# Optimization experiments

Hardware: AMD Instinct MI355X
Metric: run time of the kernel (lower is better)

## Reference

```python
import jax, jax.numpy as jnp
import numpy as np

U, I, A, D, NC = 20000, 15000, 2048, 64, 2048
N = U + I
E_AU, E_AI, E_UI, E_R = 300000, 300000, 300000, 60000


def setup_inputs() -> dict:
    keys = iter(jax.random.split(jax.random.key(0), 128))
    def rn(shape, s=0.05):
        return jax.random.normal(next(keys), shape, jnp.float32) * s
    def ru(shape):
        return jax.random.uniform(next(keys), shape, dtype=jnp.float32)
    def ri(shape, mx):
        return jax.random.randint(next(keys), shape, 0, mx)
    d = {}
    for nm in ("feature1", "feature2", "feature3", "weight1", "weight2", "weight3", "weight4", "weight5"):
        d[nm] = rn((N, D))
    d["W_review1"] = rn((D, D)); d["W_review2"] = rn((D, D))
    for i in range(1, 7):
        d["rating_emb%d" % i] = rn((5, D))
    d["W_aspect"] = rn((D, D)); d["W_aspect2"] = rn((D, D))
    d["W_count_user"] = rn((NC, D)); d["b_count_user"] = rn((D,))
    d["W_count_item"] = rn((NC, D)); d["b_count_item"] = rn((D,))
    d["aspect_fe"] = rn((A, D)); d["aspect_cau"] = rn((A, D)); d["aspect_cai"] = rn((A, D))
    d["user_cau"] = rn((U, D)); d["user_cui"] = rn((U, D))
    d["item_cai"] = rn((I, D)); d["item_ciu"] = rn((I, D))
    for i in range(1, 6):
        d["user_cui%d" % i] = rn((U, D)); d["item_ciu%d" % i] = rn((I, D))
    d["user_mask"] = ru((U,)); d["item_mask"] = ru((I,))
    d["user_aspect_count"] = ru((U, NC)); d["item_aspect_count"] = ru((I, NC))
    d["ui_review"] = rn((E_UI, D), 1.0); d["iu_review"] = rn((E_UI, D), 1.0)
    for i in range(1, 6):
        d["ui%d_review" % i] = rn((E_R, D), 1.0); d["iu%d_review" % i] = rn((E_R, D), 1.0)
    d["au_src"] = ri((E_AU,), A); d["au_dst"] = ri((E_AU,), U)
    d["ai_src"] = ri((E_AI,), A); d["ai_dst"] = ri((E_AI,), I)
    d["ui_src"] = ri((E_UI,), U); d["ui_dst"] = ri((E_UI,), I); d["ui_rating"] = ri((E_UI,), 5)
    d["iu_src"] = ri((E_UI,), I); d["iu_dst"] = ri((E_UI,), U); d["iu_rating"] = ri((E_UI,), 5)
    for i in range(1, 6):
        d["ui%d_src" % i] = ri((E_R,), U); d["ui%d_dst" % i] = ri((E_R,), I)
        d["iu%d_src" % i] = ri((E_R,), I); d["iu%d_dst" % i] = ri((E_R,), U)
    return d


def reference(feature1, feature2, feature3, weight1, weight2, weight3, weight4, weight5,
              W_review1, W_review2, rating_emb1, rating_emb2, rating_emb3, rating_emb4,
              rating_emb5, rating_emb6, W_aspect, W_aspect2, W_count_user, b_count_user,
              W_count_item, b_count_item, aspect_fe, aspect_cau, aspect_cai,
              user_cau, user_cui, user_cui1, user_cui2, user_cui3, user_cui4, user_cui5,
              user_mask, user_aspect_count, item_cai, item_ciu, item_ciu1, item_ciu2,
              item_ciu3, item_ciu4, item_ciu5, item_mask, item_aspect_count,
              ui_review, iu_review, ui1_review, ui2_review, ui3_review, ui4_review, ui5_review,
              iu1_review, iu2_review, iu3_review, iu4_review, iu5_review,
              au_src, au_dst, ai_src, ai_dst, ui_src, ui_dst, ui_rating,
              iu_src, iu_dst, iu_rating,
              ui1_src, ui1_dst, ui2_src, ui2_dst, ui3_src, ui3_dst, ui4_src, ui4_dst,
              ui5_src, ui5_dst, iu1_src, iu1_dst, iu2_src, iu2_dst, iu3_src, iu3_dst,
              iu4_src, iu4_dst, iu5_src, iu5_dst):
    sig = jax.nn.sigmoid
    cat = jnp.concatenate
    def seg(m, idx, n):
        return jax.ops.segment_sum(m, idx, num_segments=n)
    u_fe1, i_fe1 = feature1[:U], feature1[U:]
    u_fe2, i_fe2 = feature2[:U], feature2[U:]
    u_fe3, i_fe3 = feature3[:U], feature3[U:]
    mu = user_mask[:, None]; mi = item_mask[:, None]
    # --- aspect -> user/item (dropout = identity, eval mode) ---
    f_fe = aspect_fe @ W_aspect        # [A, D]
    f_fe2 = aspect_fe @ W_aspect2
    h_u = seg((f_fe * aspect_cau)[au_src], au_dst, U)
    h_i = seg((f_fe2 * aspect_cai)[ai_src], ai_dst, I)
    from_a_u = mu * (h_u * user_cau) + (1.0 - mu) * u_fe2
    from_a_i = mi * (h_i * item_cai) + (1.0 - mi) * i_fe2
    # --- rating-gated pass over from_a ---
    h_i = seg((from_a_u * user_cui)[ui_src] * sig(rating_emb1[ui_rating]), ui_dst, I)
    h_u = seg((from_a_i * item_ciu)[iu_src] * sig(rating_emb2[iu_rating]), iu_dst, U)
    user_item_senti_fe = cat([h_u * user_cui, h_i * item_ciu], 0)
    # --- aspect-count pass ---
    ac_u = user_aspect_count @ W_count_user + b_count_user
    ac_i = item_aspect_count @ W_count_item + b_count_item
    ac_u = mu * (ac_u * user_cau) + (1.0 - mu) * u_fe3
    ac_i = mi * (ac_i * item_cai) + (1.0 - mi) * i_fe3
    h_i = seg((ac_u * user_cui)[ui_src] * sig(rating_emb3[ui_rating]), ui_dst, I)
    h_u = seg((ac_i * item_ciu)[iu_src] * sig(rating_emb4[iu_rating]), iu_dst, U)
    user_item_count_fe = cat([h_u * user_cui, h_i * item_ciu], 0)
    # --- per-rating relations ---
    ws = [weight1, weight2, weight3, weight4, weight5]
    cuis = [user_cui1, user_cui2, user_cui3, user_cui4, user_cui5]
    cius = [item_ciu1, item_ciu2, item_ciu3, item_ciu4, item_ciu5]
    ui_e = [(ui1_src, ui1_dst, ui1_review), (ui2_src, ui2_dst, ui2_review),
            (ui3_src, ui3_dst, ui3_review), (ui4_src, ui4_dst, ui4_review),
            (ui5_src, ui5_dst, ui5_review)]
    iu_e = [(iu1_src, iu1_dst, iu1_review), (iu2_src, iu2_dst, iu2_review),
            (iu3_src, iu3_dst, iu3_review), (iu4_src, iu4_dst, iu4_review),
            (iu5_src, iu5_dst, iu5_review)]
    fe5_parts, re_parts = [], []
    for w, cui_k, ciu_k, (us, ud, urv), (isrc, idst, irv) in zip(ws, cuis, cius, ui_e, iu_e):
        re_ui = urv @ W_review1        # [E_R, D]
        re_iu = irv @ W_review2
        wu, wi = w[:U], w[U:]
        h_ik = seg((wu[us] + re_ui) * cui_k[us], ud, I)
        h_uk = seg((wi[isrc] + re_iu) * ciu_k[isrc], idst, U)
        fe5_parts.append(cat([h_uk * cui_k, h_ik * ciu_k], 0))
        h_ir = seg(re_ui * cui_k[us], ud, I)
        h_ur = seg(re_iu * ciu_k[isrc], idst, U)
        re_parts.append(cat([h_ur * cui_k, h_ir * ciu_k], 0))
    user_item_fe5 = cat(fe5_parts, -1)   # [N, 5*D]
    user_item_re = cat(re_parts, -1)
    # --- base-feature pass ---
    h_i = seg((u_fe1 * user_cui)[ui_src] * sig(rating_emb5[ui_rating]), ui_dst, I)
    h_u = seg((i_fe1 * item_ciu)[iu_src] * sig(rating_emb6[iu_rating]), iu_dst, U)
    user_item_fe = cat([h_u * user_cui, h_i * item_ciu], 0)
    return (user_item_senti_fe, user_item_count_fe, user_item_fe, user_item_fe5, user_item_re)
```

## Files before the change

### kernel.cpp

```cpp
#include <hip/hip_runtime.h>
#include <cstddef>

#define U_CNT 20000
#define I_CNT 15000
#define N_CNT 35000
#define A_CNT 2048
#define NC_K  2048
#define EAU   300000
#define EUI   300000
#define ER    60000
#define NLIST 14

__device__ __forceinline__ float4 ld4(const float* p){ return *reinterpret_cast<const float4*>(p); }
__device__ __forceinline__ void st4(float* p, float4 v){ *reinterpret_cast<float4*>(p) = v; }
__device__ __forceinline__ float4 mul4(float4 a, float4 b){ return make_float4(a.x*b.x, a.y*b.y, a.z*b.z, a.w*b.w); }
__device__ __forceinline__ float4 add4(float4 a, float4 b){ return make_float4(a.x+b.x, a.y+b.y, a.z+b.z, a.w+b.w); }
__device__ __forceinline__ float4 fmas4(float s, float4 b, float4 c){
  return make_float4(fmaf(s,b.x,c.x), fmaf(s,b.y,c.y), fmaf(s,b.z,c.z), fmaf(s,b.w,c.w));
}

__global__ __launch_bounds__(256) void fill_m1(int4* __restrict__ p, int n4)
{
  int gid = blockIdx.x*256 + threadIdx.x;
  if (gid < n4) p[gid] = make_int4(-1,-1,-1,-1);
}

__device__ __forceinline__ void gemm_core(
    const float* __restrict__ A, int lda, int M, int r0,
    const float* __restrict__ W, int k0base, int kcount,
    float* __restrict__ smem, float4* accs)
{
  float (*As)[36] = (float (*)[36])smem;
  float (*Ws)[64] = (float (*)[64])(smem + 64*36);
  const int t = threadIdx.x;
  const int ty = t >> 4, tx = t & 15;
  float4 acc0 = make_float4(0,0,0,0), acc1 = acc0, acc2 = acc0, acc3 = acc0;
  for (int k0 = k0base; k0 < k0base + kcount; k0 += 32) {
    __syncthreads();
    #pragma unroll
    for (int i = 0; i < 2; ++i) {
      int f = t + i*256;
      int row = f >> 3, caa = (f & 7) << 2;
      float4 v = make_float4(0.f,0.f,0.f,0.f);
      int r = r0 + row;
      if (r < M) v = ld4(&A[(size_t)r*lda + k0 + caa]);
      st4(&As[row][caa], v);
      int kk = f >> 4, cb = (f & 15) << 2;
      st4(&Ws[kk][cb], ld4(&W[(size_t)(k0+kk)*64 + cb]));
    }
    __syncthreads();
    #pragma unroll
    for (int kk = 0; kk < 32; kk += 4) {
      float4 a0 = ld4(&As[ty*4+0][kk]);
      float4 a1 = ld4(&As[ty*4+1][kk]);
      float4 a2 = ld4(&As[ty*4+2][kk]);
      float4 a3 = ld4(&As[ty*4+3][kk]);
      float a0v[4] = {a0.x,a0.y,a0.z,a0.w};
      float a1v[4] = {a1.x,a1.y,a1.z,a1.w};
      float a2v[4] = {a2.x,a2.y,a2.z,a2.w};
      float a3v[4] = {a3.x,a3.y,a3.z,a3.w};
      #pragma unroll
      for (int j = 0; j < 4; ++j) {
        float4 wv = ld4(&Ws[kk+j][tx<<2]);
        acc0 = fmas4(a0v[j], wv, acc0);
        acc1 = fmas4(a1v[j], wv, acc1);
        acc2 = fmas4(a2v[j], wv, acc2);
        acc3 = fmas4(a3v[j], wv, acc3);
      }
    }
  }
  accs[0]=acc0; accs[1]=acc1; accs[2]=acc2; accs[3]=acc3;
}

struct Mega1Args {
  int e_sp, e_build, e_k64, e_fe1c, split;
  const float* emb[6]; float* sigt;
  const float* f1; const float* cui; const float* ciu; float* fe1c;
  const float* spA[2]; const float* spW[2]; float* spPart[2]; int spM[2];
  const float* kA[12]; const float* kW[12]; const float* kMul[12]; float* kC[12]; int kM[12];
  const int* bsrc[NLIST]; const int* bdst[NLIST];
  const int* rat2; const int* rat3;
  int2* node[NLIST]; int* head[NLIST];
};

__global__ __launch_bounds__(256, 8) void mega1(Mega1Args a)
{
  __shared__ float smem[64*36 + 32*64];
  int b = blockIdx.x, t = threadIdx.x;
  if (b < a.e_sp) {
    int nb0 = a.split*313;
    int side, sp, bx;
    if (b < nb0) { side = 0; sp = b/313; bx = b%313; }
    else         { int b2 = b-nb0; side = 1; sp = b2/235; bx = b2%235; }
    int M = a.spM[side];
    int r0 = bx*64;
    int kchunk = NC_K / a.split;
    float4 accs[4];
    gemm_core(a.spA[side], NC_K, M, r0, a.spW[side], sp*kchunk, kchunk, smem, accs);
    float* base = a.spPart[side] + (size_t)sp * M * 64;
    int ty = t >> 4, tx = t & 15;
    #pragma unroll
    for (int i = 0; i < 4; ++i) {
      int r = r0 + ty*4 + i;
      if (r < M) st4(&base[(size_t)r*64 + (tx<<2)], accs[i]);
    }
    return;
  }
  if (b < a.e_build) {
    int local = b - a.e_sp;
    int li, bx;
    if (local < 4*1172) { li = local/1172; bx = local%1172; }
    else { int l2 = local - 4*1172; li = 4 + l2/235; bx = l2%235; }
    int E = (li < 4) ? EAU : ER;
    int i = bx*256 + t;
    if (i < E) {
      int d = a.bdst[li][i];
      int pay = a.bsrc[li][i];
      if (li == 2) pay |= a.rat2[i] << 20;
      else if (li == 3) pay |= a.rat3[i] << 20;
      int prev = atomicExch(&a.head[li][d], i);
      a.node[li][i] = make_int2(prev, pay);
    }
    return;
  }
  if (b < a.e_k64) {
    int local = b - a.e_build;
    int z, bx;
    if (local < 64) { z = local/32; bx = local%32; }
    else { int l2 = local - 64; z = 2 + l2/938; bx = l2%938; }
    int M = a.kM[z];
    int r0 = bx*64;
    float4 accs[4];
    gemm_core(a.kA[z], 64, M, r0, a.kW[z], 0, 64, smem, accs);
    const float* mulp = a.kMul[z];
    float* C = a.kC[z];
    int ty = t >> 4, tx = t & 15;
    #pragma unroll
    for (int i = 0; i < 4; ++i) {
      int r = r0 + ty*4 + i;
      if (r < M) {
        float4 v = accs[i];
        size_t o = (size_t)r*64 + (tx<<2);
        if (mulp) v = mul4(v, ld4(&mulp[o]));
        st4(&C[o], v);
      }
    }
    return;
  }
  if (b < a.e_fe1c) {
    int gid = (b - a.e_k64)*256 + t;
    if (gid < N_CNT*16) {
      int n = gid >> 4, q = (gid & 15) << 2;
      size_t o = (size_t)n*64 + q;
      float4 v = ld4(&a.f1[o]);
      float4 c = (n < U_CNT) ? ld4(&a.cui[o]) : ld4(&a.ciu[(size_t)(n-U_CNT)*64 + q]);
      st4(&a.fe1c[o], mul4(v, c));
    }
    return;
  }
  {
    int gid = (b - a.e_fe1c)*256 + t;
    if (gid < 6*320) {
      int k = gid/320, j = gid%320;
      a.sigt[gid] = 1.f/(1.f + __expf(-a.emb[k][j]));
    }
  }
}

#define FE5Z 10
struct Mega2Args {
  int split;
  const int* f_head[FE5Z]; const int2* f_node[FE5Z];
  const float* f_re[FE5Z]; const float* f_w[FE5Z]; const float* f_cui[FE5Z];
  const float* f_cmul[FE5Z]; float* f_outA[FE5Z]; float* f_outB[FE5Z]; int f_n[FE5Z];
  const int* gb_head[2]; const int2* gb_node[2];
  const float* gb_msg[2]; const float* gb_mask[2]; const float* gb_ca[2];
  const float* gb_fe[2]; const float* gb_cui[2]; float* gb_out[2]; int gb_n[2];
  const float* part[2]; int M[2];
  const float* bias[2]; const float* mask[2];
  const float* ca[2]; const float* fe[2]; const float* cui[2]; float* outb[2];
};

__global__ __launch_bounds__(256) void mega2(Mega2Args a)
{
  int b = blockIdx.x, t = threadIdx.x;
  int q = (t & 15) << 2;
  const int B_FE5 = 5*1250 + 5*938;
  if (b < B_FE5) {
    int z, bx;
    if (b < 6250) { z = 2*(b/1250) + 1; bx = b%1250; }
    else { int l2 = b - 6250; z = 2*(l2/938); bx = l2%938; }
    int d = bx*16 + (t >> 4);
    if (d >= a.f_n[z]) return;
    const int2* __restrict__ node = a.f_node[z];
    const float* __restrict__ re = a.f_re[z];
    const float* __restrict__ w = a.f_w[z];
    const float* __restrict__ cuiS = a.f_cui[z];
    float4 a0 = make_float4(0,0,0,0), a1 = a0;
    for (int cur = a.f_head[z][d]; cur >= 0; ) {
      int2 nd = node[cur];
      int e = cur;
      cur = nd.x;
      int s = nd.y;
      float4 rv = ld4(&re[(size_t)e*64 + q]);
      float4 cv = ld4(&cuiS[(size_t)s*64 + q]);
      float4 wv = ld4(&w[(size_t)s*64 + q]);
      a0 = add4(a0, mul4(add4(wv, rv), cv));
      a1 = add4(a1, mul4(rv, cv));
    }
    float4 c = ld4(&a.f_cmul[z][(size_t)d*64 + q]);
    size_t o = (size_t)d*320 + q;
    st4(&a.f_outA[z][o], mul4(a0, c));
    st4(&a.f_outB[z][o], mul4(a1, c));
    return;
  }
  int local = b - B_FE5;
  if (local < 2188) {
    int side = (local >= 1250);
    int bx = side ? (local - 1250) : local;
    int d = bx*16 + (t >> 4);
    if (d >= a.gb_n[side]) return;
    const int2* __restrict__ node = a.gb_node[side];
    const float* __restrict__ msg = a.gb_msg[side];
    float4 acc = make_float4(0,0,0,0);
    for (int cur = a.gb_head[side][d]; cur >= 0; ) {
      int2 nd = node[cur];
      cur = nd.x;
      acc = add4(acc, ld4(&msg[(size_t)nd.y*64 + q]));
    }
    size_t o = (size_t)d*64 + q;
    float m = a.gb_mask[side][d], im = 1.f - m;
    float4 cav = ld4(&a.gb_ca[side][o]), fev = ld4(&a.gb_fe[side][o]), cv = ld4(&a.gb_cui[side][o]);
    st4(&a.gb_out[side][o], make_float4((m*(acc.x*cav.x) + im*fev.x)*cv.x,
                                        (m*(acc.y*cav.y) + im*fev.y)*cv.y,
                                        (m*(acc.z*cav.z) + im*fev.z)*cv.z,
                                        (m*(acc.w*cav.w) + im*fev.w)*cv.w));
    return;
  }
  local -= 2188;
  int side = (local >= 1250);
  int gid = (side ? (local - 1250) : local)*256 + t;
  int M = a.M[side];
  if (gid >= M*16) return;
  int n = gid >> 4;
  float4 acc = ld4(&a.bias[side][q]);
  const float* part = a.part[side];
  for (int s = 0; s < a.split; ++s)
    acc = add4(acc, ld4(&part[((size_t)s*M + n)*64 + q]));
  size_t o = (size_t)n*64 + q;
  float m = a.mask[side][n], im = 1.f - m;
  float4 cav = ld4(&a.ca[side][o]), fev = ld4(&a.fe[side][o]), cv = ld4(&a.cui[side][o]);
  st4(&a.outb[side][o], make_float4((m*(acc.x*cav.x) + im*fev.x)*cv.x,
                                    (m*(acc.y*cav.y) + im*fev.y)*cv.y,
                                    (m*(acc.z*cav.z) + im*fev.z)*cv.z,
                                    (m*(acc.w*cav.w) + im*fev.w)*cv.w));
}

struct Mega3Args {
  int e_g3i;
  const int* head[2]; const int2* node[2];
  const float* msgA[2]; const float* msgB[2]; const float* msgC[2];
  const float* sigA[2]; const float* sigB[2]; const float* sigC[2];
  const float* cmul[2]; float* outA[2]; float* outB[2]; float* outC[2]; int n[2];
};

__global__ __launch_bounds__(256) void mega3(Mega3Args a)
{
  int b = blockIdx.x, t = threadIdx.x;
  int side = (b >= a.e_g3i);
  int bx = side ? (b - a.e_g3i) : b;
  int d = bx*16 + (t >> 4);
  if (d >= a.n[side]) return;
  int q = (t & 15) << 2;
  const int2* __restrict__ node = a.node[side];
  const float* __restrict__ msgA = a.msgA[side];
  const float* __restrict__ msgB = a.msgB[side];
  const float* __restrict__ msgC = a.msgC[side];
  const float* __restrict__ sigA = a.sigA[side];
  const float* __restrict__ sigB = a.sigB[side];
  const float* __restrict__ sigC = a.sigC[side];
  float4 a0 = make_float4(0,0,0,0), a1 = a0, a2 = a0;
  for (int cur = a.head[side][d]; cur >= 0; ) {
    int2 nd = node[cur];
    cur = nd.x;
    int s = nd.y & 0xFFFFF;
    int r = nd.y >> 20;
    size_t so = (size_t)s*64 + q;
    int ro = r*64 + q;
    a0 = add4(a0, mul4(ld4(&msgA[so]), ld4(&sigA[ro])));
    a1 = add4(a1, mul4(ld4(&msgB[so]), ld4(&sigB[ro])));
    a2 = add4(a2, mul4(ld4(&msgC[so]), ld4(&sigC[ro])));
  }
  size_t o = (size_t)d*64 + q;
  float4 c = ld4(&a.cmul[side][o]);
  st4(&a.outA[side][o], mul4(a0, c));
  st4(&a.outB[side][o], mul4(a1, c));
  st4(&a.outC[side][o], mul4(a2, c));
}

extern "C" void kernel_launch(void* const* d_in, const int* in_sizes, int n_in,
                              void* d_out, int out_size, void* d_ws, size_t ws_size,
                              hipStream_t stream)
{
  (void)in_sizes; (void)n_in; (void)out_size;
  auto F = [&](int i){ return (const float*)d_in[i]; };
  auto Ix = [&](int i){ return (const int*)d_in[i]; };

  const float* feature1 = F(0);
  const float* feature2 = F(1);
  const float* feature3 = F(2);
  const float* weightK[5]   = {F(3),F(4),F(5),F(6),F(7)};
  const float* W_review1 = F(8);
  const float* W_review2 = F(9);
  const float* rating_emb[6] = {F(10),F(11),F(12),F(13),F(14),F(15)};
  const float* W_aspect  = F(16);
  const float* W_aspect2 = F(17);
  const float* W_count_user = F(18);
  const float* b_count_user = F(19);
  const float* W_count_item = F(20);
  const float* b_count_item = F(21);
  const float* aspect_fe  = F(22);
  const float* aspect_cau = F(23);
  const float* aspect_cai = F(24);
  const float* user_cau = F(25);
  const float* user_cui = F(26);
  const float* item_cai = F(27);
  const float* item_ciu = F(28);
  const float* user_cuiK[5] = {F(29),F(31),F(33),F(35),F(37)};
  const float* item_ciuK[5] = {F(30),F(32),F(34),F(36),F(38)};
  const float* user_mask = F(39);
  const float* item_mask = F(40);
  const float* user_aspect_count = F(41);
  const float* item_aspect_count = F(42);
  const float* uiK_review[5] = {F(45),F(47),F(49),F(51),F(53)};
  const float* iuK_review[5] = {F(46),F(48),F(50),F(52),F(54)};
  const int* au_src = Ix(55); const int* au_dst = Ix(56);
  const int* ai_src = Ix(57); const int* ai_dst = Ix(58);
  const int* ui_src = Ix(59); const int* ui_dst = Ix(60); const int* ui_rating = Ix(61);
  const int* iu_src = Ix(62); const int* iu_dst = Ix(63); const int* iu_rating = Ix(64);
  const int* uiK_src[5] = {Ix(65),Ix(69),Ix(73),Ix(77),Ix(81)};
  const int* uiK_dst[5] = {Ix(66),Ix(70),Ix(74),Ix(78),Ix(82)};
  const int* iuK_src[5] = {Ix(67),Ix(71),Ix(75),Ix(79),Ix(83)};
  const int* iuK_dst[5] = {Ix(68),Ix(72),Ix(76),Ix(80),Ix(84)};

  float* out  = (float*)d_out;
  float* out2 = out + (size_t)N_CNT*64;
  float* out3 = out + 2*(size_t)N_CNT*64;
  float* out4 = out + 3*(size_t)N_CNT*64;
  float* out5 = out + 8*(size_t)N_CNT*64;

  float* ws = (float*)d_ws;
  size_t off = 0;
  auto alloc = [&](size_t n){ float* p = ws + off; off += (n + 3) & ~(size_t)3; return p; };
  float* sigt   = alloc(6*320);
  float* msg_au = alloc((size_t)A_CNT*64);
  float* msg_ai = alloc((size_t)A_CNT*64);
  float* h_u_a  = alloc((size_t)U_CNT*64);
  float* h_i_a  = alloc((size_t)I_CNT*64);
  float* g_u    = alloc((size_t)U_CNT*64);
  float* g_i    = alloc((size_t)I_CNT*64);
  float* fe1c   = alloc((size_t)N_CNT*64);

  const int* l_src[NLIST] = {au_src, ai_src, ui_src, iu_src,
                             uiK_src[0],uiK_src[1],uiK_src[2],uiK_src[3],uiK_src[4],
                             iuK_src[0],iuK_src[1],iuK_src[2],iuK_src[3],iuK_src[4]};
  const int* l_dst[NLIST] = {au_dst, ai_dst, ui_dst, iu_dst,
                             uiK_dst[0],uiK_dst[1],uiK_dst[2],uiK_dst[3],uiK_dst[4],
                             iuK_dst[0],iuK_dst[1],iuK_dst[2],iuK_dst[3],iuK_dst[4]};
  int l_E[NLIST]    = {EAU,EAU,EUI,EUI, ER,ER,ER,ER,ER, ER,ER,ER,ER,ER};
  int l_nseg[NLIST] = {U_CNT,I_CNT,I_CNT,U_CNT, I_CNT,I_CNT,I_CNT,I_CNT,I_CNT,
                       U_CNT,U_CNT,U_CNT,U_CNT,U_CNT};

  int* ibase = (int*)(ws + off);
  int* lhead[NLIST]; int2* lnode[NLIST];
  size_t io = 0;
  for (int l = 0; l < NLIST; ++l) { lhead[l] = ibase + io; io += l_nseg[l]; }
  size_t head_ints = io;
  for (int l = 0; l < NLIST; ++l) { lnode[l] = (int2*)(ibase + io); io += 2*(size_t)l_E[l]; }
  off += (io + 3) & ~(size_t)3;

  const size_t reN = (size_t)ER*64;
  int SPLIT = 4;
  while (SPLIT > 1 && (off + (size_t)SPLIT*N_CNT*64 + 10*reN) * 4 > ws_size) SPLIT >>= 1;
  float* part_u = ws + off;
  float* part_i = part_u + (size_t)SPLIT*U_CNT*64;
  float* rebase = part_u + (size_t)SPLIT*N_CNT*64;
  float* reb[10];
  for (int j = 0; j < 10; ++j) reb[j] = rebase + (size_t)j*reN;

  fill_m1<<<(int)((head_ints/4 + 255)/256), 256, 0, stream>>>((int4*)ibase, (int)(head_ints/4));

  Mega1Args a1;
  const int B_SP    = SPLIT*313 + SPLIT*235;
  const int B_BUILD = 4*1172 + 10*235;
  const int B_K64   = 2*32 + 10*938;
  const int B_FE1C  = (N_CNT*16 + 255)/256;
  const int B_SIG   = 8;
  a1.e_sp    = B_SP;
  a1.e_build = B_SP + B_BUILD;
  a1.e_k64   = a1.e_build + B_K64;
  a1.e_fe1c  = a1.e_k64 + B_FE1C;
  a1.split   = SPLIT;
  for (int k = 0; k < 6; ++k) a1.emb[k] = rating_emb[k];
  a1.sigt = sigt;
  a1.f1 = feature1; a1.cui = user_cui; a1.ciu = item_ciu; a1.fe1c = fe1c;
  a1.spA[0] = user_aspect_count; a1.spW[0] = W_count_user; a1.spPart[0] = part_u; a1.spM[0] = U_CNT;
  a1.spA[1] = item_aspect_count; a1.spW[1] = W_count_item; a1.spPart[1] = part_i; a1.spM[1] = I_CNT;
  a1.kA[0]=aspect_fe; a1.kW[0]=W_aspect;  a1.kMul[0]=aspect_cau; a1.kC[0]=msg_au; a1.kM[0]=A_CNT;
  a1.kA[1]=aspect_fe; a1.kW[1]=W_aspect2; a1.kMul[1]=aspect_cai; a1.kC[1]=msg_ai; a1.kM[1]=A_CNT;
  for (int k = 0; k < 5; ++k) {
    a1.kA[2+k]=uiK_review[k]; a1.kW[2+k]=W_review1; a1.kMul[2+k]=nullptr; a1.kC[2+k]=reb[k];   a1.kM[2+k]=ER;
    a1.kA[7+k]=iuK_review[k]; a1.kW[7+k]=W_review2; a1.kMul[7+k]=nullptr; a1.kC[7+k]=reb[5+k]; a1.kM[7+k]=ER;
  }
  for (int l = 0; l < NLIST; ++l) {
    a1.bsrc[l]=l_src[l]; a1.bdst[l]=l_dst[l];
    a1.node[l]=lnode[l]; a1.head[l]=lhead[l];
  }
  a1.rat2 = ui_rating; a1.rat3 = iu_rating;
  mega1<<<a1.e_fe1c + B_SIG, 256, 0, stream>>>(a1);

  Mega2Args a2;
  a2.split = SPLIT;
  for (int k = 0; k < 5; ++k) {
    int z = 2*k;
    a2.f_head[z]=lhead[4+k]; a2.f_node[z]=lnode[4+k];
    a2.f_re[z]=reb[k]; a2.f_w[z]=weightK[k]; a2.f_cui[z]=user_cuiK[k]; a2.f_cmul[z]=item_ciuK[k];
    a2.f_outA[z]=out4 + (size_t)U_CNT*320 + (size_t)k*64;
    a2.f_outB[z]=out5 + (size_t)U_CNT*320 + (size_t)k*64;
    a2.f_n[z]=I_CNT;
    a2.f_head[z+1]=lhead[9+k]; a2.f_node[z+1]=lnode[9+k];
    a2.f_re[z+1]=reb[5+k]; a2.f_w[z+1]=weightK[k] + (size_t)U_CNT*64;
    a2.f_cui[z+1]=item_ciuK[k]; a2.f_cmul[z+1]=user_cuiK[k];
    a2.f_outA[z+1]=out4 + (size_t)k*64;
    a2.f_outB[z+1]=out5 + (size_t)k*64;
    a2.f_n[z+1]=U_CNT;
  }
  a2.gb_head[0]=lhead[0]; a2.gb_node[0]=lnode[0]; a2.gb_msg[0]=msg_au;
  a2.gb_mask[0]=user_mask; a2.gb_ca[0]=user_cau; a2.gb_fe[0]=feature2;
  a2.gb_cui[0]=user_cui; a2.gb_out[0]=h_u_a; a2.gb_n[0]=U_CNT;
  a2.gb_head[1]=lhead[1]; a2.gb_node[1]=lnode[1]; a2.gb_msg[1]=msg_ai;
  a2.gb_mask[1]=item_mask; a2.gb_ca[1]=item_cai; a2.gb_fe[1]=feature2 + (size_t)U_CNT*64;
  a2.gb_cui[1]=item_ciu; a2.gb_out[1]=h_i_a; a2.gb_n[1]=I_CNT;
  a2.part[0]=part_u; a2.M[0]=U_CNT; a2.bias[0]=b_count_user; a2.mask[0]=user_mask;
  a2.ca[0]=user_cau; a2.fe[0]=feature3; a2.cui[0]=user_cui; a2.outb[0]=g_u;
  a2.part[1]=part_i; a2.M[1]=I_CNT; a2.bias[1]=b_count_item; a2.mask[1]=item_mask;
  a2.ca[1]=item_cai; a2.fe[1]=feature3 + (size_t)U_CNT*64; a2.cui[1]=item_ciu; a2.outb[1]=g_i;
  const int B_M2 = (5*1250 + 5*938) + 2188 + 2188;
  mega2<<<B_M2, 256, 0, stream>>>(a2);

  Mega3Args a3;
  a3.e_g3i = 938;
  a3.head[0]=lhead[2]; a3.node[0]=lnode[2];
  a3.msgA[0]=h_u_a; a3.msgB[0]=g_u; a3.msgC[0]=fe1c;
  a3.sigA[0]=sigt + 0*320; a3.sigB[0]=sigt + 2*320; a3.sigC[0]=sigt + 4*320;
  a3.cmul[0]=item_ciu;
  a3.outA[0]=out + (size_t)U_CNT*64; a3.outB[0]=out2 + (size_t)U_CNT*64; a3.outC[0]=out3 + (size_t)U_CNT*64;
  a3.n[0]=I_CNT;
  a3.head[1]=lhead[3]; a3.node[1]=lnode[3];
  a3.msgA[1]=h_i_a; a3.msgB[1]=g_i; a3.msgC[1]=fe1c + (size_t)U_CNT*64;
  a3.sigA[1]=sigt + 1*320; a3.sigB[1]=sigt + 3*320; a3.sigC[1]=sigt + 5*320;
  a3.cmul[1]=user_cui;
  a3.outA[1]=out; a3.outB[1]=out2; a3.outC[1]=out3;
  a3.n[1]=U_CNT;
  mega3<<<938 + 1250, 256, 0, stream>>>(a3);
}
```

Before: 459.9 us.

## Use bf16x3 split MFMA for dense GEMMs with prepacked hi/lo weights

Replaces the shared-memory fp32 FMA GEMM core in mega1 with MFMA 16x16x32 bf16 instructions, using a three-term hi/lo bf16 split to keep close to fp32 accuracy. Weights are converted once per call in a new prep kernel, fused with the -1 fill, into an MFMA-friendly packed layout. Activations are split on the fly from global memory with no LDS staging, and the launch bounds are relaxed. The aim is to cut ALU time in the large count GEMM (U/I x 2048 x 64) and the review projections. The cost is three MFMAs per tile, scalar strided output stores, and a small loss of accuracy from dropping the lo*lo term.

Result: no change. 458.1 us (-0.4%).

```diff
diff --git a/kernel.cpp b/kernel.cpp
--- a/kernel.cpp
+++ b/kernel.cpp
@@ -11,81 +11,103 @@
 #define ER    60000
 #define NLIST 14
 
+typedef __attribute__((ext_vector_type(8))) short bf16x8;
+typedef __attribute__((ext_vector_type(4))) float f32x4;
+
 __device__ __forceinline__ float4 ld4(const float* p){ return *reinterpret_cast<const float4*>(p); }
 __device__ __forceinline__ void st4(float* p, float4 v){ *reinterpret_cast<float4*>(p) = v; }
 __device__ __forceinline__ float4 mul4(float4 a, float4 b){ return make_float4(a.x*b.x, a.y*b.y, a.z*b.z, a.w*b.w); }
 __device__ __forceinline__ float4 add4(float4 a, float4 b){ return make_float4(a.x+b.x, a.y+b.y, a.z+b.z, a.w+b.w); }
-__device__ __forceinline__ float4 fmas4(float s, float4 b, float4 c){
-  return make_float4(fmaf(s,b.x,c.x), fmaf(s,b.y,c.y), fmaf(s,b.z,c.z), fmaf(s,b.w,c.w));
-}
-
-__global__ __launch_bounds__(256) void fill_m1(int4* __restrict__ p, int n4)
-{
-  int gid = blockIdx.x*256 + threadIdx.x;
-  if (gid < n4) p[gid] = make_int4(-1,-1,-1,-1);
-}
-
-__device__ __forceinline__ void gemm_core(
+
+__device__ __forceinline__ void cvt_hilo(float4 a, float4 b, bf16x8& h, bf16x8& l)
+{
+  float v0=a.x,v1=a.y,v2=a.z,v3=a.w,v4=b.x,v5=b.y,v6=b.z,v7=b.w;
+  float vv[8] = {v0,v1,v2,v3,v4,v5,v6,v7};
+  #pragma unroll
+  for (int j = 0; j < 8; ++j) {
+    unsigned int bi = __float_as_uint(vv[j]);
+    h[j] = (short)(bi >> 16);
+    float hf = __uint_as_float(bi & 0xffff0000u);
+    l[j] = (short)(__float_as_uint(vv[j] - hf) >> 16);
+  }
+}
+
+__device__ __forceinline__ void gemm_mfma(
     const float* __restrict__ A, int lda, int M, int r0,
-    const float* __restrict__ W, int k0base, int kcount,
-    float* __restrict__ smem, float4* accs)
-{
-  float (*As)[36] = (float (*)[36])smem;
-  float (*Ws)[64] = (float (*)[64])(smem + 64*36);
+    const unsigned short* __restrict__ Wh, const unsigned short* __restrict__ Wl,
+    int s0, int nsteps, f32x4* acc)
+{
   const int t = threadIdx.x;
-  const int ty = t >> 4, tx = t & 15;
-  float4 acc0 = make_float4(0,0,0,0), acc1 = acc0, acc2 = acc0, acc3 = acc0;
-  for (int k0 = k0base; k0 < k0base + kcount; k0 += 32) {
-    __syncthreads();
+  const int w = t >> 6, l = t & 63;
+  const int lr = l & 15, g = l >> 4;
+  const int row = r0 + w*16 + lr;
+  const bool rowok = row < M;
+  const float* arow = A + (size_t)row*lda;
+  for (int s = s0; s < s0 + nsteps; ++s) {
+    float4 a0 = make_float4(0.f,0.f,0.f,0.f), a1 = a0;
+    if (rowok) {
+      a0 = ld4(arow + s*32 + g*8);
+      a1 = ld4(arow + s*32 + g*8 + 4);
+    }
+    bf16x8 ah, al;
+    cvt_hilo(a0, a1, ah, al);
+    const unsigned short* bh_base = Wh + (size_t)(s*4 + g)*64*8;
+    const unsigned short* bl_base = Wl + (size_t)(s*4 + g)*64*8;
     #pragma unroll
-    for (int i = 0; i < 2; ++i) {
-      int f = t + i*256;
-      int row = f >> 3, caa = (f & 7) << 2;
-      float4 v = make_float4(0.f,0.f,0.f,0.f);
-      int r = r0 + row;
-      if (r < M) v = ld4(&A[(size_t)r*lda + k0 + caa]);
-      st4(&As[row][caa], v);
-      int kk = f >> 4, cb = (f & 15) << 2;
-      st4(&Ws[kk][cb], ld4(&W[(size_t)(k0+kk)*64 + cb]));
-    }
-    __syncthreads();
-    #pragma unroll
-    for (int kk = 0; kk < 32; kk += 4) {
-      float4 a0 = ld4(&As[ty*4+0][kk]);
-      float4 a1 = ld4(&As[ty*4+1][kk]);
-      float4 a2 = ld4(&As[ty*4+2][kk]);
-      float4 a3 = ld4(&As[ty*4+3][kk]);
-      float a0v[4] = {a0.x,a0.y,a0.z,a0.w};
-      float a1v[4] = {a1.x,a1.y,a1.z,a1.w};
-      float a2v[4] = {a2.x,a2.y,a2.z,a2.w};
-      float a3v[4] = {a3.x,a3.y,a3.z,a3.w};
-      #pragma unroll
-      for (int j = 0; j < 4; ++j) {
-        float4 wv = ld4(&Ws[kk+j][tx<<2]);
-        acc0 = fmas4(a0v[j], wv, acc0);
-        acc1 = fmas4(a1v[j], wv, acc1);
-        acc2 = fmas4(a2v[j], wv, acc2);
-        acc3 = fmas4(a3v[j], wv, acc3);
-      }
-    }
-  }
-  accs[0]=acc0; accs[1]=acc1; accs[2]=acc2; accs[3]=acc3;
+    for (int cb = 0; cb < 4; ++cb) {
+      bf16x8 bh = *reinterpret_cast<const bf16x8*>(bh_base + (cb*16 + lr)*8);
+      bf16x8 bl = *reinterpret_cast<const bf16x8*>(bl_base + (cb*16 + lr)*8);
+      acc[cb] = __builtin_amdgcn_mfma_f32_16x16x32_bf16(ah, bh, acc[cb], 0, 0, 0);
+      acc[cb] = __builtin_amdgcn_mfma_f32_16x16x32_bf16(ah, bl, acc[cb], 0, 0, 0);
+      acc[cb] = __builtin_amdgcn_mfma_f32_16x16x32_bf16(al, bh, acc[cb], 0, 0, 0);
+    }
+  }
+}
+
+struct PrepArgs {
+  int e_fill;
+  int4* fillp; int fill_n4;
+  const float* wsrc[6]; unsigned short* whi[6]; unsigned short* wlo[6];
+  int welems[6]; int wblocks[6];
+};
+
+__global__ __launch_bounds__(256) void prep(PrepArgs a)
+{
+  int b = blockIdx.x, t = threadIdx.x;
+  if (b < a.e_fill) {
+    int gid = b*256 + t;
+    if (gid < a.fill_n4) a.fillp[gid] = make_int4(-1,-1,-1,-1);
+    return;
+  }
+  int local = b - a.e_fill;
+  int z = 0;
+  while (z < 5 && local >= a.wblocks[z]) { local -= a.wblocks[z]; ++z; }
+  int e = local*256 + t;
+  if (e >= a.welems[z]) return;
+  int k = e >> 6, c = e & 63;
+  int idx = ((k >> 3)*64 + c)*8 + (k & 7);
+  float v = a.wsrc[z][e];
+  unsigned int bi = __float_as_uint(v);
+  a.whi[z][idx] = (unsigned short)(bi >> 16);
+  float hf = __uint_as_float(bi & 0xffff0000u);
+  a.wlo[z][idx] = (unsigned short)(__float_as_uint(v - hf) >> 16);
 }
 
 struct Mega1Args {
   int e_sp, e_build, e_k64, e_fe1c, split;
   const float* emb[6]; float* sigt;
   const float* f1; const float* cui; const float* ciu; float* fe1c;
-  const float* spA[2]; const float* spW[2]; float* spPart[2]; int spM[2];
-  const float* kA[12]; const float* kW[12]; const float* kMul[12]; float* kC[12]; int kM[12];
+  const float* spA[2]; const unsigned short* spWh[2]; const unsigned short* spWl[2];
+  float* spPart[2]; int spM[2];
+  const float* kA[12]; const unsigned short* kWh[12]; const unsigned short* kWl[12];
+  const float* kMul[12]; float* kC[12]; int kM[12];
   const int* bsrc[NLIST]; const int* bdst[NLIST];
   const int* rat2; const int* rat3;
   int2* node[NLIST]; int* head[NLIST];
 };
 
-__global__ __launch_bounds__(256, 8) void mega1(Mega1Args a)
-{
-  __shared__ float smem[64*36 + 32*64];
+__global__ __launch_bounds__(256, 4) void mega1(Mega1Args a)
+{
   int b = blockIdx.x, t = threadIdx.x;
   if (b < a.e_sp) {
     int nb0 = a.split*313;
@@ -94,16 +116,21 @@
     else         { int b2 = b-nb0; side = 1; sp = b2/235; bx = b2%235; }
     int M = a.spM[side];
     int r0 = bx*64;
-    int kchunk = NC_K / a.split;
-    float4 accs[4];
-    gemm_core(a.spA[side], NC_K, M, r0, a.spW[side], sp*kchunk, kchunk, smem, accs);
+    int spsteps = NC_K/(a.split*32);
+    f32x4 acc[4];
+    #pragma unroll
+    for (int cb = 0; cb < 4; ++cb) acc[cb] = (f32x4){0.f,0.f,0.f,0.f};
+    gemm_mfma(a.spA[side], NC_K, M, r0, a.spWh[side], a.spWl[side], sp*spsteps, spsteps, acc);
     float* base = a.spPart[side] + (size_t)sp * M * 64;
-    int ty = t >> 4, tx = t & 15;
+    int l = t & 63, w = t >> 6;
+    int lr = l & 15, g = l >> 4;
     #pragma unroll
-    for (int i = 0; i < 4; ++i) {
-      int r = r0 + ty*4 + i;
-      if (r < M) st4(&base[(size_t)r*64 + (tx<<2)], accs[i]);
-    }
+    for (int cb = 0; cb < 4; ++cb)
+      #pragma unroll
+      for (int i = 0; i < 4; ++i) {
+        int r = r0 + w*16 + g*4 + i;
+        if (r < M) base[(size_t)r*64 + cb*16 + lr] = acc[cb][i];
+      }
     return;
   }
   if (b < a.e_build) {
@@ -130,21 +157,26 @@
     else { int l2 = local - 64; z = 2 + l2/938; bx = l2%938; }
     int M = a.kM[z];
     int r0 = bx*64;
-    float4 accs[4];
-    gemm_core(a.kA[z], 64, M, r0, a.kW[z], 0, 64, smem, accs);
+    f32x4 acc[4];
+    #pragma unroll
+    for (int cb = 0; cb < 4; ++cb) acc[cb] = (f32x4){0.f,0.f,0.f,0.f};
+    gemm_mfma(a.kA[z], 64, M, r0, a.kWh[z], a.kWl[z], 0, 2, acc);
     const float* mulp = a.kMul[z];
     float* C = a.kC[z];
-    int ty = t >> 4, tx = t & 15;
+    int l = t & 63, w = t >> 6;
+    int lr = l & 15, g = l >> 4;
     #pragma unroll
-    for (int i = 0; i < 4; ++i) {
-      int r = r0 + ty*4 + i;
-      if (r < M) {
-        float4 v = accs[i];
-        size_t o = (size_t)r*64 + (tx<<2);
-        if (mulp) v = mul4(v, ld4(&mulp[o]));
-        st4(&C[o], v);
+    for (int cb = 0; cb < 4; ++cb)
+      #pragma unroll
+      for (int i = 0; i < 4; ++i) {
+        int r = r0 + w*16 + g*4 + i;
+        if (r < M) {
+          size_t o = (size_t)r*64 + cb*16 + lr;
+          float v = acc[cb][i];
+          if (mulp) v *= mulp[o];
+          C[o] = v;
+        }
       }
-    }
     return;
   }
   if (b < a.e_fe1c) {
@@ -361,6 +393,12 @@
   float* g_i    = alloc((size_t)I_CNT*64);
   float* fe1c   = alloc((size_t)N_CNT*64);
 
+  const size_t WP_USH = 2*131072 + 4*4096;
+  float* wpf = alloc(WP_USH);
+  unsigned short* wph = (unsigned short*)wpf;
+  unsigned short* wpl = wph + WP_USH;
+  const size_t o_cu = 0, o_ci = 131072, o_a1 = 262144, o_a2 = 266240, o_r1 = 270336, o_r2 = 274432;
+
   const int* l_src[NLIST] = {au_src, ai_src, ui_src, iu_src,
                              uiK_src[0],uiK_src[1],uiK_src[2],uiK_src[3],uiK_src[4],
                              iuK_src[0],iuK_src[1],iuK_src[2],iuK_src[3],iuK_src[4]};
@@ -388,7 +426,22 @@
   float* reb[10];
   for (int j = 0; j < 10; ++j) reb[j] = rebase + (size_t)j*reN;
 
-  fill_m1<<<(int)((head_ints/4 + 255)/256), 256, 0, stream>>>((int4*)ibase, (int)(head_ints/4));
+  PrepArgs ap;
+  ap.e_fill = (int)((head_ints/4 + 255)/256);
+  ap.fillp = (int4*)ibase; ap.fill_n4 = (int)(head_ints/4);
+  const float* wsrcs[6] = {W_count_user, W_count_item, W_aspect, W_aspect2, W_review1, W_review2};
+  const size_t woffs[6] = {o_cu, o_ci, o_a1, o_a2, o_r1, o_r2};
+  const int welems[6] = {131072, 131072, 4096, 4096, 4096, 4096};
+  int prep_blocks = ap.e_fill;
+  for (int z = 0; z < 6; ++z) {
+    ap.wsrc[z] = wsrcs[z];
+    ap.whi[z] = wph + woffs[z];
+    ap.wlo[z] = wpl + woffs[z];
+    ap.welems[z] = welems[z];
+    ap.wblocks[z] = (welems[z] + 255)/256;
+    prep_blocks += ap.wblocks[z];
+  }
+  prep<<<prep_blocks, 256, 0, stream>>>(ap);
 
   Mega1Args a1;
   const int B_SP    = SPLIT*313 + SPLIT*235;
@@ -404,13 +457,17 @@
   for (int k = 0; k < 6; ++k) a1.emb[k] = rating_emb[k];
   a1.sigt = sigt;
   a1.f1 = feature1; a1.cui = user_cui; a1.ciu = item_ciu; a1.fe1c = fe1c;
-  a1.spA[0] = user_aspect_count; a1.spW[0] = W_count_user; a1.spPart[0] = part_u; a1.spM[0] = U_CNT;
-  a1.spA[1] = item_aspect_count; a1.spW[1] = W_count_item; a1.spPart[1] = part_i; a1.spM[1] = I_CNT;
-  a1.kA[0]=aspect_fe; a1.kW[0]=W_aspect;  a1.kMul[0]=aspect_cau; a1.kC[0]=msg_au; a1.kM[0]=A_CNT;
-  a1.kA[1]=aspect_fe; a1.kW[1]=W_aspect2; a1.kMul[1]=aspect_cai; a1.kC[1]=msg_ai; a1.kM[1]=A_CNT;
+  a1.spA[0] = user_aspect_count; a1.spWh[0] = wph + o_cu; a1.spWl[0] = wpl + o_cu;
+  a1.spPart[0] = part_u; a1.spM[0] = U_CNT;
+  a1.spA[1] = item_aspect_count; a1.spWh[1] = wph + o_ci; a1.spWl[1] = wpl + o_ci;
+  a1.spPart[1] = part_i; a1.spM[1] = I_CNT;
+  a1.kA[0]=aspect_fe; a1.kWh[0]=wph+o_a1; a1.kWl[0]=wpl+o_a1; a1.kMul[0]=aspect_cau; a1.kC[0]=msg_au; a1.kM[0]=A_CNT;
+  a1.kA[1]=aspect_fe; a1.kWh[1]=wph+o_a2; a1.kWl[1]=wpl+o_a2; a1.kMul[1]=aspect_cai; a1.kC[1]=msg_ai; a1.kM[1]=A_CNT;
   for (int k = 0; k < 5; ++k) {
-    a1.kA[2+k]=uiK_review[k]; a1.kW[2+k]=W_review1; a1.kMul[2+k]=nullptr; a1.kC[2+k]=reb[k];   a1.kM[2+k]=ER;
-    a1.kA[7+k]=iuK_review[k]; a1.kW[7+k]=W_review2; a1.kMul[7+k]=nullptr; a1.kC[7+k]=reb[5+k]; a1.kM[7+k]=ER;
+    a1.kA[2+k]=uiK_review[k]; a1.kWh[2+k]=wph+o_r1; a1.kWl[2+k]=wpl+o_r1;
+    a1.kMul[2+k]=nullptr; a1.kC[2+k]=reb[k];   a1.kM[2+k]=ER;
+    a1.kA[7+k]=iuK_review[k]; a1.kWh[7+k]=wph+o_r2; a1.kWl[7+k]=wpl+o_r2;
+    a1.kMul[7+k]=nullptr; a1.kC[7+k]=reb[5+k]; a1.kM[7+k]=ER;
   }
   for (int l = 0; l < NLIST; ++l) {
     a1.bsrc[l]=l_src[l]; a1.bdst[l]=l_dst[l];
```

## Drop split-K count GEMM, fuse its epilogue, store review projections in bf16

Applied to the files above, without the earlier changes.

The count-feature GEMM (K=2048) no longer splits K into partial buffers reduced in mega2. Each block now runs the full K loop and applies bias, mask, aspect multiply and cui multiply in its own epilogue. This removes the partial-sum traffic and the separate reduction phase, but the work now sits in far fewer blocks, each with a long serial K loop. The review projection outputs are also written as bf16 and widened in the gather loop, halving their memory traffic at the cost of precision.

Result: slower. 481.1 us (+4.6%).

```diff
diff --git a/kernel.cpp b/kernel.cpp
--- a/kernel.cpp
+++ b/kernel.cpp
@@ -18,11 +18,13 @@
 __device__ __forceinline__ float4 fmas4(float s, float4 b, float4 c){
   return make_float4(fmaf(s,b.x,c.x), fmaf(s,b.y,c.y), fmaf(s,b.z,c.z), fmaf(s,b.w,c.w));
 }
-
-__global__ __launch_bounds__(256) void fill_m1(int4* __restrict__ p, int n4)
-{
-  int gid = blockIdx.x*256 + threadIdx.x;
-  if (gid < n4) p[gid] = make_int4(-1,-1,-1,-1);
+__device__ __forceinline__ unsigned short f2bf(float x){
+  unsigned u = __float_as_uint(x);
+  u += 0x7fffu + ((u >> 16) & 1u);
+  return (unsigned short)(u >> 16);
+}
+__device__ __forceinline__ float bf2f(unsigned short s){
+  return __uint_as_float(((unsigned)s) << 16);
 }
 
 __device__ __forceinline__ void gemm_core(
@@ -72,12 +74,21 @@
   accs[0]=acc0; accs[1]=acc1; accs[2]=acc2; accs[3]=acc3;
 }
 
+__global__ __launch_bounds__(256) void fill_m1(int4* __restrict__ p, int n4)
+{
+  int gid = blockIdx.x*256 + threadIdx.x;
+  if (gid < n4) p[gid] = make_int4(-1,-1,-1,-1);
+}
+
 struct Mega1Args {
-  int e_sp, e_build, e_k64, e_fe1c, split;
+  int e_sp, e_build, e_k64a, e_k64r, e_fe1c;
   const float* emb[6]; float* sigt;
   const float* f1; const float* cui; const float* ciu; float* fe1c;
-  const float* spA[2]; const float* spW[2]; float* spPart[2]; int spM[2];
-  const float* kA[12]; const float* kW[12]; const float* kMul[12]; float* kC[12]; int kM[12];
+  const float* spA[2]; const float* spW[2]; int spM[2];
+  const float* spBias[2]; const float* spMask[2];
+  const float* spCa[2]; const float* spFe[2]; const float* spCui[2]; float* spOut[2];
+  const float* aA[2]; const float* aW[2]; const float* aMul[2]; float* aC[2];
+  const float* rA[10]; const float* rW[10]; unsigned short* rC[10];
   const int* bsrc[NLIST]; const int* bdst[NLIST];
   const int* rat2; const int* rat3;
   int2* node[NLIST]; int* head[NLIST];
@@ -87,22 +98,28 @@
 {
   __shared__ float smem[64*36 + 32*64];
   int b = blockIdx.x, t = threadIdx.x;
+  const int ty = t >> 4, tx = t & 15;
   if (b < a.e_sp) {
-    int nb0 = a.split*313;
-    int side, sp, bx;
-    if (b < nb0) { side = 0; sp = b/313; bx = b%313; }
-    else         { int b2 = b-nb0; side = 1; sp = b2/235; bx = b2%235; }
+    int side = (b >= 313);
+    int bx = side ? (b - 313) : b;
     int M = a.spM[side];
     int r0 = bx*64;
-    int kchunk = NC_K / a.split;
     float4 accs[4];
-    gemm_core(a.spA[side], NC_K, M, r0, a.spW[side], sp*kchunk, kchunk, smem, accs);
-    float* base = a.spPart[side] + (size_t)sp * M * 64;
-    int ty = t >> 4, tx = t & 15;
+    gemm_core(a.spA[side], NC_K, M, r0, a.spW[side], 0, NC_K, smem, accs);
+    float4 bv = ld4(&a.spBias[side][tx<<2]);
     #pragma unroll
     for (int i = 0; i < 4; ++i) {
       int r = r0 + ty*4 + i;
-      if (r < M) st4(&base[(size_t)r*64 + (tx<<2)], accs[i]);
+      if (r < M) {
+        size_t o = (size_t)r*64 + (tx<<2);
+        float4 v = add4(accs[i], bv);
+        float m = a.spMask[side][r], im = 1.f - m;
+        float4 cav = ld4(&a.spCa[side][o]), fev = ld4(&a.spFe[side][o]), cv = ld4(&a.spCui[side][o]);
+        st4(&a.spOut[side][o], make_float4((m*(v.x*cav.x) + im*fev.x)*cv.x,
+                                           (m*(v.y*cav.y) + im*fev.y)*cv.y,
+                                           (m*(v.z*cav.z) + im*fev.z)*cv.z,
+                                           (m*(v.w*cav.w) + im*fev.w)*cv.w));
+      }
     }
     return;
   }
@@ -123,32 +140,43 @@
     }
     return;
   }
-  if (b < a.e_k64) {
+  if (b < a.e_k64a) {
     int local = b - a.e_build;
-    int z, bx;
-    if (local < 64) { z = local/32; bx = local%32; }
-    else { int l2 = local - 64; z = 2 + l2/938; bx = l2%938; }
-    int M = a.kM[z];
+    int z = local/32, bx = local%32;
     int r0 = bx*64;
     float4 accs[4];
-    gemm_core(a.kA[z], 64, M, r0, a.kW[z], 0, 64, smem, accs);
-    const float* mulp = a.kMul[z];
-    float* C = a.kC[z];
-    int ty = t >> 4, tx = t & 15;
+    gemm_core(a.aA[z], 64, A_CNT, r0, a.aW[z], 0, 64, smem, accs);
+    const float* mulp = a.aMul[z];
+    float* C = a.aC[z];
     #pragma unroll
     for (int i = 0; i < 4; ++i) {
       int r = r0 + ty*4 + i;
-      if (r < M) {
-        float4 v = accs[i];
-        size_t o = (size_t)r*64 + (tx<<2);
-        if (mulp) v = mul4(v, ld4(&mulp[o]));
-        st4(&C[o], v);
+      size_t o = (size_t)r*64 + (tx<<2);
+      st4(&C[o], mul4(accs[i], ld4(&mulp[o])));
+    }
+    return;
+  }
+  if (b < a.e_k64r) {
+    int local = b - a.e_k64a;
+    int z = local/938, bx = local%938;
+    int r0 = bx*64;
+    float4 accs[4];
+    gemm_core(a.rA[z], 64, ER, r0, a.rW[z], 0, 64, smem, accs);
+    unsigned short* C = a.rC[z];
+    #pragma unroll
+    for (int i = 0; i < 4; ++i) {
+      int r = r0 + ty*4 + i;
+      if (r < ER) {
+        ushort4 o4;
+        o4.x = f2bf(accs[i].x); o4.y = f2bf(accs[i].y);
+        o4.z = f2bf(accs[i].z); o4.w = f2bf(accs[i].w);
+        *reinterpret_cast<ushort4*>(&C[(size_t)r*64 + (tx<<2)]) = o4;
       }
     }
     return;
   }
   if (b < a.e_fe1c) {
-    int gid = (b - a.e_k64)*256 + t;
+    int gid = (b - a.e_k64r)*256 + t;
     if (gid < N_CNT*16) {
       int n = gid >> 4, q = (gid & 15) << 2;
       size_t o = (size_t)n*64 + q;
@@ -169,16 +197,12 @@
 
 #define FE5Z 10
 struct Mega2Args {
-  int split;
   const int* f_head[FE5Z]; const int2* f_node[FE5Z];
-  const float* f_re[FE5Z]; const float* f_w[FE5Z]; const float* f_cui[FE5Z];
+  const unsigned short* f_re[FE5Z]; const float* f_w[FE5Z]; const float* f_cui[FE5Z];
   const float* f_cmul[FE5Z]; float* f_outA[FE5Z]; float* f_outB[FE5Z]; int f_n[FE5Z];
   const int* gb_head[2]; const int2* gb_node[2];
   const float* gb_msg[2]; const float* gb_mask[2]; const float* gb_ca[2];
   const float* gb_fe[2]; const float* gb_cui[2]; float* gb_out[2]; int gb_n[2];
-  const float* part[2]; int M[2];
-  const float* bias[2]; const float* mask[2];
-  const float* ca[2]; const float* fe[2]; const float* cui[2]; float* outb[2];
 };
 
 __global__ __launch_bounds__(256) void mega2(Mega2Args a)
@@ -193,7 +217,7 @@
     int d = bx*16 + (t >> 4);
     if (d >= a.f_n[z]) return;
     const int2* __restrict__ node = a.f_node[z];
-    const float* __restrict__ re = a.f_re[z];
+    const unsigned short* __restrict__ re = a.f_re[z];
     const float* __restrict__ w = a.f_w[z];
     const float* __restrict__ cuiS = a.f_cui[z];
     float4 a0 = make_float4(0,0,0,0), a1 = a0;
@@ -202,7 +226,8 @@
       int e = cur;
       cur = nd.x;
       int s = nd.y;
-      float4 rv = ld4(&re[(size_t)e*64 + q]);
+      ushort4 r4 = *reinterpret_cast<const ushort4*>(&re[(size_t)e*64 + q]);
+      float4 rv = make_float4(bf2f(r4.x), bf2f(r4.y), bf2f(r4.z), bf2f(r4.w));
       float4 cv = ld4(&cuiS[(size_t)s*64 + q]);
       float4 wv = ld4(&w[(size_t)s*64 + q]);
       a0 = add4(a0, mul4(add4(wv, rv), cv));
@@ -215,7 +240,7 @@
     return;
   }
   int local = b - B_FE5;
-  if (local < 2188) {
+  {
     int side = (local >= 1250);
     int bx = side ? (local - 1250) : local;
     int d = bx*16 + (t >> 4);
@@ -235,25 +260,7 @@
                                         (m*(acc.y*cav.y) + im*fev.y)*cv.y,
                                         (m*(acc.z*cav.z) + im*fev.z)*cv.z,
                                         (m*(acc.w*cav.w) + im*fev.w)*cv.w));
-    return;
-  }
-  local -= 2188;
-  int side = (local >= 1250);
-  int gid = (side ? (local - 1250) : local)*256 + t;
-  int M = a.M[side];
-  if (gid >= M*16) return;
-  int n = gid >> 4;
-  float4 acc = ld4(&a.bias[side][q]);
-  const float* part = a.part[side];
-  for (int s = 0; s < a.split; ++s)
-    acc = add4(acc, ld4(&part[((size_t)s*M + n)*64 + q]));
-  size_t o = (size_t)n*64 + q;
-  float m = a.mask[side][n], im = 1.f - m;
-  float4 cav = ld4(&a.ca[side][o]), fev = ld4(&a.fe[side][o]), cv = ld4(&a.cui[side][o]);
-  st4(&a.outb[side][o], make_float4((m*(acc.x*cav.x) + im*fev.x)*cv.x,
-                                    (m*(acc.y*cav.y) + im*fev.y)*cv.y,
-                                    (m*(acc.z*cav.z) + im*fev.z)*cv.z,
-                                    (m*(acc.w*cav.w) + im*fev.w)*cv.w));
+  }
 }
 
 struct Mega3Args {
@@ -302,7 +309,7 @@
                               void* d_out, int out_size, void* d_ws, size_t ws_size,
                               hipStream_t stream)
 {
-  (void)in_sizes; (void)n_in; (void)out_size;
+  (void)in_sizes; (void)n_in; (void)out_size; (void)ws_size;
   auto F = [&](int i){ return (const float*)d_in[i]; };
   auto Ix = [&](int i){ return (const int*)d_in[i]; };
 
@@ -361,6 +368,11 @@
   float* g_i    = alloc((size_t)I_CNT*64);
   float* fe1c   = alloc((size_t)N_CNT*64);
 
+  const size_t reUSH = (size_t)ER*64;
+  float* rebf = alloc(10*reUSH/2);
+  unsigned short* rebb[10];
+  for (int j = 0; j < 10; ++j) rebb[j] = (unsigned short*)rebf + (size_t)j*reUSH;
+
   const int* l_src[NLIST] = {au_src, ai_src, ui_src, iu_src,
                              uiK_src[0],uiK_src[1],uiK_src[2],uiK_src[3],uiK_src[4],
                              iuK_src[0],iuK_src[1],iuK_src[2],iuK_src[3],iuK_src[4]};
@@ -379,38 +391,34 @@
   for (int l = 0; l < NLIST; ++l) { lnode[l] = (int2*)(ibase + io); io += 2*(size_t)l_E[l]; }
   off += (io + 3) & ~(size_t)3;
 
-  const size_t reN = (size_t)ER*64;
-  int SPLIT = 4;
-  while (SPLIT > 1 && (off + (size_t)SPLIT*N_CNT*64 + 10*reN) * 4 > ws_size) SPLIT >>= 1;
-  float* part_u = ws + off;
-  float* part_i = part_u + (size_t)SPLIT*U_CNT*64;
-  float* rebase = part_u + (size_t)SPLIT*N_CNT*64;
-  float* reb[10];
-  for (int j = 0; j < 10; ++j) reb[j] = rebase + (size_t)j*reN;
-
   fill_m1<<<(int)((head_ints/4 + 255)/256), 256, 0, stream>>>((int4*)ibase, (int)(head_ints/4));
 
   Mega1Args a1;
-  const int B_SP    = SPLIT*313 + SPLIT*235;
+  const int B_SP    = 313 + 235;
   const int B_BUILD = 4*1172 + 10*235;
-  const int B_K64   = 2*32 + 10*938;
+  const int B_K64A  = 64;
+  const int B_K64R  = 10*938;
   const int B_FE1C  = (N_CNT*16 + 255)/256;
   const int B_SIG   = 8;
   a1.e_sp    = B_SP;
   a1.e_build = B_SP + B_BUILD;
-  a1.e_k64   = a1.e_build + B_K64;
-  a1.e_fe1c  = a1.e_k64 + B_FE1C;
-  a1.split   = SPLIT;
+  a1.e_k64a  = a1.e_build + B_K64A;
+  a1.e_k64r  = a1.e_k64a + B_K64R;
+  a1.e_fe1c  = a1.e_k64r + B_FE1C;
   for (int k = 0; k < 6; ++k) a1.emb[k] = rating_emb[k];
   a1.sigt = sigt;
   a1.f1 = feature1; a1.cui = user_cui; a1.ciu = item_ciu; a1.fe1c = fe1c;
-  a1.spA[0] = user_aspect_count; a1.spW[0] = W_count_user; a1.spPart[0] = part_u; a1.spM[0] = U_CNT;
-  a1.spA[1] = item_aspect_count; a1.spW[1] = W_count_item; a1.spPart[1] = part_i; a1.spM[1] = I_CNT;
-  a1.kA[0]=aspect_fe; a1.kW[0]=W_aspect;  a1.kMul[0]=aspect_cau; a1.kC[0]=msg_au; a1.kM[0]=A_CNT;
-  a1.kA[1]=aspect_fe; a1.kW[1]=W_aspect2; a1.kMul[1]=aspect_cai; a1.kC[1]=msg_ai; a1.kM[1]=A_CNT;
+  a1.spA[0] = user_aspect_count; a1.spW[0] = W_count_user; a1.spM[0] = U_CNT;
+  a1.spBias[0] = b_count_user; a1.spMask[0] = user_mask;
+  a1.spCa[0] = user_cau; a1.spFe[0] = feature3; a1.spCui[0] = user_cui; a1.spOut[0] = g_u;
+  a1.spA[1] = item_aspect_count; a1.spW[1] = W_count_item; a1.spM[1] = I_CNT;
+  a1.spBias[1] = b_count_item; a1.spMask[1] = item_mask;
+  a1.spCa[1] = item_cai; a1.spFe[1] = feature3 + (size_t)U_CNT*64; a1.spCui[1] = item_ciu; a1.spOut[1] = g_i;
+  a1.aA[0]=aspect_fe; a1.aW[0]=W_aspect;  a1.aMul[0]=aspect_cau; a1.aC[0]=msg_au;
+  a1.aA[1]=aspect_fe; a1.aW[1]=W_aspect2; a1.aMul[1]=aspect_cai; a1.aC[1]=msg_ai;
   for (int k = 0; k < 5; ++k) {
-    a1.kA[2+k]=uiK_review[k]; a1.kW[2+k]=W_review1; a1.kMul[2+k]=nullptr; a1.kC[2+k]=reb[k];   a1.kM[2+k]=ER;
-    a1.kA[7+k]=iuK_review[k]; a1.kW[7+k]=W_review2; a1.kMul[7+k]=nullptr; a1.kC[7+k]=reb[5+k]; a1.kM[7+k]=ER;
+    a1.rA[k]   = uiK_review[k]; a1.rW[k]   = W_review1; a1.rC[k]   = rebb[k];
+    a1.rA[5+k] = iuK_review[k]; a1.rW[5+k] = W_review2; a1.rC[5+k] = rebb[5+k];
   }
   for (int l = 0; l < NLIST; ++l) {
     a1.bsrc[l]=l_src[l]; a1.bdst[l]=l_dst[l];
@@ -420,16 +428,15 @@
   mega1<<<a1.e_fe1c + B_SIG, 256, 0, stream>>>(a1);
 
   Mega2Args a2;
-  a2.split = SPLIT;
   for (int k = 0; k < 5; ++k) {
     int z = 2*k;
     a2.f_head[z]=lhead[4+k]; a2.f_node[z]=lnode[4+k];
-    a2.f_re[z]=reb[k]; a2.f_w[z]=weightK[k]; a2.f_cui[z]=user_cuiK[k]; a2.f_cmul[z]=item_ciuK[k];
+    a2.f_re[z]=rebb[k]; a2.f_w[z]=weightK[k]; a2.f_cui[z]=user_cuiK[k]; a2.f_cmul[z]=item_ciuK[k];
     a2.f_outA[z]=out4 + (size_t)U_CNT*320 + (size_t)k*64;
     a2.f_outB[z]=out5 + (size_t)U_CNT*320 + (size_t)k*64;
     a2.f_n[z]=I_CNT;
     a2.f_head[z+1]=lhead[9+k]; a2.f_node[z+1]=lnode[9+k];
-    a2.f_re[z+1]=reb[5+k]; a2.f_w[z+1]=weightK[k] + (size_t)U_CNT*64;
+    a2.f_re[z+1]=rebb[5+k]; a2.f_w[z+1]=weightK[k] + (size_t)U_CNT*64;
     a2.f_cui[z+1]=item_ciuK[k]; a2.f_cmul[z+1]=user_cuiK[k];
     a2.f_outA[z+1]=out4 + (size_t)k*64;
     a2.f_outB[z+1]=out5 + (size_t)k*64;
@@ -441,11 +448,7 @@
   a2.gb_head[1]=lhead[1]; a2.gb_node[1]=lnode[1]; a2.gb_msg[1]=msg_ai;
   a2.gb_mask[1]=item_mask; a2.gb_ca[1]=item_cai; a2.gb_fe[1]=feature2 + (size_t)U_CNT*64;
   a2.gb_cui[1]=item_ciu; a2.gb_out[1]=h_i_a; a2.gb_n[1]=I_CNT;
-  a2.part[0]=part_u; a2.M[0]=U_CNT; a2.bias[0]=b_count_user; a2.mask[0]=user_mask;
-  a2.ca[0]=user_cau; a2.fe[0]=feature3; a2.cui[0]=user_cui; a2.outb[0]=g_u;
-  a2.part[1]=part_i; a2.M[1]=I_CNT; a2.bias[1]=b_count_item; a2.mask[1]=item_mask;
-  a2.ca[1]=item_cai; a2.fe[1]=feature3 + (size_t)U_CNT*64; a2.cui[1]=item_ciu; a2.outb[1]=g_i;
-  const int B_M2 = (5*1250 + 5*938) + 2188 + 2188;
+  const int B_M2 = (5*1250 + 5*938) + 2188;
   mega2<<<B_M2, 256, 0, stream>>>(a2);
 
   Mega3Args a3;
```
